# Kernel optimization log

Hardware: AMD Instinct MI355X
Metric: run time of the kernel (lower is better)

The kernel has to match this reference:

```python
import jax, jax.numpy as jnp
import numpy as np

N_USERS = 50000
N_ENTITIES = 100000
N_FACTORS = 8
N_RELATIONS = 17  # weight has n_relations-1 = 16 rows
EMB = 64
N_EDGES = 2_000_000
NNZ = 2_000_000
SLOPE = 0.2


def setup_inputs() -> dict:
    key = jax.random.key(0)
    ks = jax.random.split(key, 16)
    inp = {
        "entity_emb": jax.random.normal(ks[0], (N_ENTITIES, EMB), jnp.float32),
        "user_emb": jax.random.normal(ks[1], (N_USERS, EMB), jnp.float32),
        "latent_emb": jax.random.normal(ks[2], (N_FACTORS, EMB), jnp.float32),
        "edge_index": jax.random.randint(ks[3], (2, N_EDGES), 0, N_ENTITIES, jnp.int32),
        "edge_type": jax.random.randint(ks[4], (N_EDGES,), 1, N_RELATIONS, jnp.int32),
        "interact_rows": jax.random.randint(ks[5], (NNZ,), 0, N_USERS, jnp.int32),
        "interact_cols": jax.random.randint(ks[6], (NNZ,), 0, N_ENTITIES, jnp.int32),
        "interact_vals": jax.random.uniform(ks[7], (NNZ,), jnp.float32),
        "weight": jax.random.normal(ks[8], (N_RELATIONS - 1, EMB), jnp.float32),
        "entity_cate_set": jax.random.randint(ks[9], (N_ENTITIES,), 1, 33, jnp.int32),
        # params (torch Linear convention: y = x @ W.T + b)
        "W_user_att": jax.random.normal(ks[10], (N_FACTORS, N_FACTORS), jnp.float32) * 0.1,
        "b_user_att": jnp.zeros((N_FACTORS,), jnp.float32),
        "W_weight_att": jax.random.normal(ks[11], (N_RELATIONS - 1, N_RELATIONS - 1), jnp.float32) * 0.1,
        "b_weight_att": jnp.zeros((N_RELATIONS - 1,), jnp.float32),
        "W1": jax.random.normal(ks[12], (EMB, EMB), jnp.float32) * 0.1,
        "b1": jnp.zeros((EMB,), jnp.float32),
        "W2": jax.random.normal(ks[13], (EMB, EMB), jnp.float32) * 0.1,
        "b2": jnp.zeros((EMB,), jnp.float32),
    }
    return inp


def _lin(x, W, b):
    return x @ W.T + b


def reference(entity_emb, user_emb, latent_emb, edge_index, edge_type,
              interact_rows, interact_cols, interact_vals, weight, entity_cate_set,
              W_user_att, b_user_att, W_weight_att, b_weight_att, W1, b1, W2, b2):
    head, tail = edge_index[0], edge_index[1]

    # KG aggregate: gather-multiply-scatter_mean (is_div=False branch)
    neigh = entity_emb[tail] * weight[edge_type - 1]            # [E, C]
    sums = jax.ops.segment_sum(neigh, head, num_segments=N_ENTITIES)
    cnt = jax.ops.segment_sum(jnp.ones((neigh.shape[0],), neigh.dtype),
                              head, num_segments=N_ENTITIES)
    entity_agg = sums / jnp.maximum(cnt, 1.0)[:, None]          # [N_ent, C]

    # user aggregate: sparse mm (COO) interact_mat @ entity_emb
    user_agg = jax.ops.segment_sum(interact_vals[:, None] * entity_emb[interact_cols],
                                   interact_rows, num_segments=N_USERS)  # [U, C]

    # user -> latent interest attention
    score_ = _lin(user_emb, W1, b1) @ _lin(latent_emb, W1, b1).T          # [U, F]
    score = jax.nn.softmax(jax.nn.leaky_relu(_lin(score_, W_user_att, b_user_att), SLOPE), axis=1)  # [U, F]

    score_rp = _lin(latent_emb, W2, b2) @ _lin(weight, W2, b2).T          # [F, R-1]
    latent_new = jax.nn.softmax(jax.nn.leaky_relu(_lin(score_rp, W_weight_att, b_weight_att), SLOPE), axis=-1) @ weight  # [F, C]

    # (disen_weight * score).sum(dim=1) == score @ latent_new
    user_agg = user_agg * (score @ latent_new) + user_agg
    return (entity_agg, user_agg, latent_new)
```

## Files before the change

### kernel.cpp

```cpp
#include <hip/hip_runtime.h>

#define N_USERS    50000
#define N_ENTITIES 100000
#define EMB        64
#define N_EDGES    2000000
#define NNZ        2000000
#define SLOPE      0.2f

#define KROWS   256
#define KSHIFT  8
#define NBK     391
#define UROWS   128
#define USHIFT  7
#define NBU     391
#define CAPK    8192
#define CAPU    7680
#define HCH     8192
#define HEPT    (HCH / 512)
#define HPB     ((N_EDGES + HCH - 1) / HCH)
#define CHK_K   8192
#define PB_K    ((N_EDGES + CHK_K - 1) / CHK_K)
#define CHK_U   4096
#define PB_U    ((NNZ + CHK_U - 1) / CHK_U)
#define NQ      (NBK + NBU)
#define ACCBLK  512

__global__ __launch_bounds__(512) void hist_both(const int* __restrict__ head,
                                                 const int* __restrict__ urows,
                                                 int* __restrict__ kgOffs,
                                                 int* __restrict__ uOffs) {
    __shared__ int lhk[NBK];
    __shared__ int lhu[NBU];
    int tid = threadIdx.x;
    for (int t = tid; t < NBK; t += 512) lhk[t] = 0;
    for (int t = tid; t < NBU; t += 512) lhu[t] = 0;
    __syncthreads();
    int base = blockIdx.x * HCH;
#pragma unroll 4
    for (int j = 0; j < HEPT; ++j) {
        int i = base + j * 512 + tid;
        if (i < N_EDGES) atomicAdd(&lhk[head[i] >> KSHIFT], 1);
        if (i < NNZ)     atomicAdd(&lhu[urows[i] >> USHIFT], 1);
    }
    __syncthreads();
    for (int t = tid; t < NBK; t += 512) { int c = lhk[t]; if (c) atomicAdd(&kgOffs[t], c); }
    for (int t = tid; t < NBU; t += 512) { int c = lhu[t]; if (c) atomicAdd(&uOffs[t], c); }
}

__global__ __launch_bounds__(512) void scan_both(int* __restrict__ kgOffs,
                                                 int* __restrict__ kgCur,
                                                 int* __restrict__ uOffs,
                                                 int* __restrict__ uCur) {
    __shared__ int tsum[512];
    int n     = (blockIdx.x == 0) ? NBK : NBU;
    int* offs = (blockIdx.x == 0) ? kgOffs : uOffs;
    int* cur  = (blockIdx.x == 0) ? kgCur  : uCur;
    int tid = threadIdx.x;
    int v = (tid < n) ? offs[tid] : 0;
    tsum[tid] = v;
    __syncthreads();
    for (int off = 1; off < 512; off <<= 1) {
        int t = (tid >= off) ? tsum[tid - off] : 0;
        __syncthreads();
        tsum[tid] += t;
        __syncthreads();
    }
    if (tid < n) { int e = tsum[tid] - v; offs[tid] = e; cur[tid] = e; }
    if (tid == n - 1) offs[n] = tsum[tid];
}

__device__ void small_dense_body(int l,
                                 const float* __restrict__ latent_emb,
                                 const float* __restrict__ weight,
                                 const float* __restrict__ W_weight_att,
                                 const float* __restrict__ b_weight_att,
                                 const float* __restrict__ W1,
                                 const float* __restrict__ b1,
                                 const float* __restrict__ W2,
                                 const float* __restrict__ b2,
                                 float* __restrict__ P_out,
                                 float* __restrict__ c_out,
                                 float* __restrict__ latent_new_out) {
    __shared__ float lat1[8 * 64];
    __shared__ float lat2[8 * 64];
    __shared__ float wl2[16 * 64];
    __shared__ float srp[8 * 16];
    __shared__ float soft[8 * 16];

    if (l < 64) {
        for (int f = 0; f < 8; ++f) {
            float a1 = b1[l], a2 = b2[l];
            for (int k = 0; k < 64; ++k) {
                float le = latent_emb[f * 64 + k];
                a1 += le * W1[l * 64 + k];
                a2 += le * W2[l * 64 + k];
            }
            lat1[f * 64 + l] = a1;
            lat2[f * 64 + l] = a2;
        }
        for (int r = 0; r < 16; ++r) {
            float a = b2[l];
            for (int k = 0; k < 64; ++k) a += weight[r * 64 + k] * W2[l * 64 + k];
            wl2[r * 64 + l] = a;
        }
    }
    __syncthreads();

    if (l < 64) {
        for (int f = 0; f < 8; ++f) {
            float p = 0.f;
            for (int d = 0; d < 64; ++d) p += W1[d * 64 + l] * lat1[f * 64 + d];
            P_out[l * 8 + f] = p;
        }
        if (l < 8) {
            float cc = 0.f;
            for (int d = 0; d < 64; ++d) cc += b1[d] * lat1[l * 64 + d];
            c_out[l] = cc;
        }
        for (int idx = l; idx < 128; idx += 64) {
            int f = idx >> 4, r = idx & 15;
            float a = 0.f;
            for (int d = 0; d < 64; ++d) a += lat2[f * 64 + d] * wl2[r * 64 + d];
            srp[idx] = a;
        }
    }
    __syncthreads();

    if (l < 8) {
        int f = l;
        float att[16];
        float mx = -1e30f;
        for (int k = 0; k < 16; ++k) {
            float a = b_weight_att[k];
            for (int j = 0; j < 16; ++j) a += srp[f * 16 + j] * W_weight_att[k * 16 + j];
            a = a > 0.f ? a : SLOPE * a;
            att[k] = a;
            mx = fmaxf(mx, a);
        }
        float s = 0.f;
        for (int k = 0; k < 16; ++k) { att[k] = expf(att[k] - mx); s += att[k]; }
        float inv = 1.f / s;
        for (int k = 0; k < 16; ++k) soft[f * 16 + k] = att[k] * inv;
    }
    __syncthreads();

    if (l < 64) {
        for (int f = 0; f < 8; ++f) {
            float a = 0.f;
            for (int r = 0; r < 16; ++r) a += soft[f * 16 + r] * weight[r * 64 + l];
            latent_new_out[f * 64 + l] = a;
        }
    }
}

__global__ void small_dense(const float* __restrict__ latent_emb,
                            const float* __restrict__ weight,
                            const float* __restrict__ W_weight_att,
                            const float* __restrict__ b_weight_att,
                            const float* __restrict__ W1,
                            const float* __restrict__ b1,
                            const float* __restrict__ W2,
                            const float* __restrict__ b2,
                            float* __restrict__ P_out,
                            float* __restrict__ c_out,
                            float* __restrict__ latent_new_out) {
    small_dense_body(threadIdx.x, latent_emb, weight, W_weight_att, b_weight_att,
                     W1, b1, W2, b2, P_out, c_out, latent_new_out);
}

__global__ __launch_bounds__(512) void scatter_both(const int* __restrict__ head,
                                                    const int* __restrict__ tail,
                                                    const int* __restrict__ etype,
                                                    int* __restrict__ kgCur,
                                                    int* __restrict__ kgPay,
                                                    const int* __restrict__ urows,
                                                    const int* __restrict__ ucols,
                                                    const float* __restrict__ uvals,
                                                    int* __restrict__ uCur,
                                                    int2* __restrict__ uPay,
                                                    const float* __restrict__ latent_emb,
                                                    const float* __restrict__ weight,
                                                    const float* __restrict__ W_weight_att,
                                                    const float* __restrict__ b_weight_att,
                                                    const float* __restrict__ W1,
                                                    const float* __restrict__ b1,
                                                    const float* __restrict__ W2,
                                                    const float* __restrict__ b2,
                                                    float* __restrict__ Pbuf,
                                                    float* __restrict__ cbuf,
                                                    float* __restrict__ lat_out) {
    if (blockIdx.x == PB_K + PB_U) {
        small_dense_body(threadIdx.x, latent_emb, weight, W_weight_att,
                         b_weight_att, W1, b1, W2, b2, Pbuf, cbuf, lat_out);
        return;
    }

    __shared__ long long sp8[4096];
    __shared__ int lh[NBK];
    __shared__ int lb[NBK];
    __shared__ int lofs[NBK + 1];
    __shared__ int sc[512];
    int tid = threadIdx.x;
    bool isKg = blockIdx.x < PB_K;

    for (int t = tid; t < NBK; t += 512) lh[t] = 0;
    __syncthreads();

    if (isKg) {
        int base = blockIdx.x * CHK_K;
        int n = N_EDGES - base; if (n > CHK_K) n = CHK_K;
        int* spk = (int*)sp8;

        int kreg[CHK_K / 512];
#pragma unroll
        for (int j = 0; j < CHK_K / 512; ++j) {
            int o = j * 512 + tid;
            int h = (o < n) ? head[base + o] : -1;
            kreg[j] = h;
            if (h >= 0) atomicAdd(&lh[h >> KSHIFT], 1);
        }
        __syncthreads();
        for (int t = tid; t < NBK; t += 512)
            lb[t] = lh[t] ? atomicAdd(&kgCur[t], lh[t]) : 0;
        int v = (tid < NBK) ? lh[tid] : 0;
        sc[tid] = v;
        __syncthreads();
        for (int off = 1; off < 512; off <<= 1) {
            int t = (tid >= off) ? sc[tid - off] : 0;
            __syncthreads();
            sc[tid] += t;
            __syncthreads();
        }
        if (tid < NBK) { int e = sc[tid] - v; lofs[tid] = e; lh[tid] = e; }
        if (tid == NBK - 1) lofs[NBK] = sc[tid];
        __syncthreads();
#pragma unroll
        for (int j = 0; j < CHK_K / 512; ++j) {
            int h = kreg[j];
            if (h >= 0) {
                int i = base + j * 512 + tid;
                int p = atomicAdd(&lh[h >> KSHIFT], 1);
                spk[p] = tail[i] | ((etype[i] - 1) << 17) | ((h & (KROWS - 1)) << 21);
            }
        }
        __syncthreads();
        for (int i = tid; i < n; i += 512) {
            int lo = 0, hi = NBK;
            while (hi - lo > 1) {
                int mid = (lo + hi) >> 1;
                if (lofs[mid] <= i) lo = mid; else hi = mid;
            }
            kgPay[lb[lo] + (i - lofs[lo])] = spk[i];
        }
    } else {
        int base = (blockIdx.x - PB_K) * CHK_U;
        int n = NNZ - base; if (n > CHK_U) n = CHK_U;
        int2* spu = (int2*)sp8;

        int kreg[CHK_U / 512];
#pragma unroll
        for (int j = 0; j < CHK_U / 512; ++j) {
            int o = j * 512 + tid;
            int r = (o < n) ? urows[base + o] : -1;
            kreg[j] = r;
            if (r >= 0) atomicAdd(&lh[r >> USHIFT], 1);
        }
        __syncthreads();
        for (int t = tid; t < NBU; t += 512)
            lb[t] = lh[t] ? atomicAdd(&uCur[t], lh[t]) : 0;
        int v = (tid < NBU) ? lh[tid] : 0;
        sc[tid] = v;
        __syncthreads();
        for (int off = 1; off < 512; off <<= 1) {
            int t = (tid >= off) ? sc[tid - off] : 0;
            __syncthreads();
            sc[tid] += t;
            __syncthreads();
        }
        if (tid < NBU) { int e = sc[tid] - v; lofs[tid] = e; lh[tid] = e; }
        if (tid == NBU - 1) lofs[NBU] = sc[tid];
        __syncthreads();
#pragma unroll
        for (int j = 0; j < CHK_U / 512; ++j) {
            int r = kreg[j];
            if (r >= 0) {
                int i = base + j * 512 + tid;
                int p = atomicAdd(&lh[r >> USHIFT], 1);
                spu[p] = make_int2(ucols[i] | ((r & (UROWS - 1)) << 17),
                                   __float_as_int(uvals[i]));
            }
        }
        __syncthreads();
        for (int i = tid; i < n; i += 512) {
            int lo = 0, hi = NBU;
            while (hi - lo > 1) {
                int mid = (lo + hi) >> 1;
                if (lofs[mid] <= i) lo = mid; else hi = mid;
            }
            uPay[lb[lo] + (i - lofs[lo])] = spu[i];
        }
    }
}

__global__ __launch_bounds__(1024, 8) void acc_both(
        const int* __restrict__ kgPay, const int* __restrict__ kgOffs,
        const int2* __restrict__ uPay, const int* __restrict__ uOffs,
        const float* __restrict__ entity_emb,
        const float* __restrict__ weight,
        const float* __restrict__ user_emb,
        const float* __restrict__ P,
        const float* __restrict__ cvec,
        const float* __restrict__ W_user_att,
        const float* __restrict__ b_user_att,
        const float* __restrict__ latent_new,
        int* __restrict__ qCtr,
        float* __restrict__ ent_out,
        float* __restrict__ user_out) {
    __shared__ long long smem8[7873];
    __shared__ int sbk;
    int t = threadIdx.x, d = t & 63, wv = t >> 6;

    for (;;) {
        __syncthreads();
        if (t == 0) sbk = atomicAdd(qCtr, 1);
        __syncthreads();
        int q = sbk;
        if (q >= NQ) return;

        if (q < NBU) {
            int2* spay = (int2*)smem8;
            int* lcnt = (int*)(spay + CAPU);
            int* lofs = lcnt + UROWS;
            int* sc   = lofs + UROWS + 1;
            int bk = q;
            int start = uOffs[bk], end = uOffs[bk + 1];
            int n = end - start; if (n > CAPU) n = CAPU;

            if (t < UROWS) lcnt[t] = 0;
            __syncthreads();
            for (int i = t; i < n; i += 1024)
                atomicAdd(&lcnt[(uPay[start + i].x >> 17) & (UROWS - 1)], 1);
            __syncthreads();
            if (t < UROWS) sc[t] = lcnt[t];
            __syncthreads();
            for (int off = 1; off < UROWS; off <<= 1) {
                int v = (t < UROWS && t >= off) ? sc[t - off] : 0;
                __syncthreads();
                if (t < UROWS) sc[t] += v;
                __syncthreads();
            }
            if (t < UROWS) { int e = sc[t] - lcnt[t]; lofs[t] = e; lcnt[t] = e; }
            if (t == 0) lofs[UROWS] = n;
            __syncthreads();
            for (int i = t; i < n; i += 1024) {
                int2 v = uPay[start + i];
                int p = atomicAdd(&lcnt[(v.x >> 17) & (UROWS - 1)], 1);
                spay[p] = v;
            }
            __syncthreads();

            int rowbase = bk * UROWS;
            for (int rr = 0; rr < UROWS / 16; ++rr) {
                int r = wv * (UROWS / 16) + rr;
                int gr = rowbase + r;
                if (gr >= N_USERS) break;
                int s0 = lofs[r], e0 = lofs[r + 1];
                float acc = 0.f;
                int i = s0;
                for (; i + 7 < e0; i += 8) {
                    float a0 = 0.f, a1 = 0.f;
#pragma unroll
                    for (int u = 0; u < 8; u += 2) {
                        int2 va = spay[i + u], vb = spay[i + u + 1];
                        a0 += __int_as_float(va.y) * entity_emb[(va.x & 0x1FFFF) * EMB + d];
                        a1 += __int_as_float(vb.y) * entity_emb[(vb.x & 0x1FFFF) * EMB + d];
                    }
                    acc += a0 + a1;
                }
                for (; i < e0; ++i) {
                    int2 v = spay[i];
                    acc += __int_as_float(v.y) * entity_emb[(v.x & 0x1FFFF) * EMB + d];
                }
                for (int j = start + CAPU; j < end; ++j) {
                    int2 v = uPay[j];
                    if (((v.x >> 17) & (UROWS - 1)) == r)
                        acc += __int_as_float(v.y) * entity_emb[(v.x & 0x1FFFF) * EMB + d];
                }

                float ue = user_emb[gr * EMB + d];
                float s[8];
#pragma unroll
                for (int f = 0; f < 8; ++f) s[f] = ue * P[d * 8 + f];
#pragma unroll
                for (int off = 32; off; off >>= 1) {
#pragma unroll
                    for (int f = 0; f < 8; ++f) s[f] += __shfl_xor(s[f], off, 64);
                }
#pragma unroll
                for (int f = 0; f < 8; ++f) s[f] += cvec[f];
                float att[8];
                float mx = -1e30f;
#pragma unroll
                for (int k = 0; k < 8; ++k) {
                    float a = b_user_att[k];
#pragma unroll
                    for (int j = 0; j < 8; ++j) a += s[j] * W_user_att[k * 8 + j];
                    a = a > 0.f ? a : SLOPE * a;
                    att[k] = a;
                    mx = fmaxf(mx, a);
                }
                float sum = 0.f;
#pragma unroll
                for (int k = 0; k < 8; ++k) { att[k] = __expf(att[k] - mx); sum += att[k]; }
                float inv = 1.f / sum;
                float g = 0.f;
#pragma unroll
                for (int f = 0; f < 8; ++f) g += att[f] * inv * latent_new[f * EMB + d];
                user_out[gr * EMB + d] = acc * (1.f + g);
            }
        } else {
            int* spay = (int*)smem8;
            int* lcnt = spay + CAPK;
            int* lofs = lcnt + KROWS;
            int* sc   = lofs + KROWS + 1;
            int bk = q - NBU;
            int start = kgOffs[bk], end = kgOffs[bk + 1];
            int n = end - start; if (n > CAPK) n = CAPK;

            if (t < KROWS) lcnt[t] = 0;
            __syncthreads();
            for (int i = t; i < n; i += 1024)
                atomicAdd(&lcnt[(kgPay[start + i] >> 21) & (KROWS - 1)], 1);
            __syncthreads();
            if (t < KROWS) sc[t] = lcnt[t];
            __syncthreads();
            for (int off = 1; off < KROWS; off <<= 1) {
                int v = (t < KROWS && t >= off) ? sc[t - off] : 0;
                __syncthreads();
                if (t < KROWS) sc[t] += v;
                __syncthreads();
            }
            if (t < KROWS) { int e = sc[t] - lcnt[t]; lofs[t] = e; lcnt[t] = e; }
            if (t == 0) lofs[KROWS] = n;
            __syncthreads();
            for (int i = t; i < n; i += 1024) {
                int v = kgPay[start + i];
                int p = atomicAdd(&lcnt[(v >> 21) & (KROWS - 1)], 1);
                spay[p] = v;
            }
            __syncthreads();

            int rowbase = bk * KROWS;
            for (int rr = 0; rr < KROWS / 16; ++rr) {
                int r = wv * (KROWS / 16) + rr;
                int gr = rowbase + r;
                if (gr >= N_ENTITIES) break;
                int s0 = lofs[r], e0 = lofs[r + 1];
                int cnt = e0 - s0;
                float acc = 0.f;
                int i = s0;
                for (; i + 7 < e0; i += 8) {
                    float a0 = 0.f, a1 = 0.f;
#pragma unroll
                    for (int u = 0; u < 8; u += 2) {
                        int va = spay[i + u], vb = spay[i + u + 1];
                        a0 += entity_emb[(va & 0x1FFFF) * EMB + d] * weight[((va >> 17) & 15) * EMB + d];
                        a1 += entity_emb[(vb & 0x1FFFF) * EMB + d] * weight[((vb >> 17) & 15) * EMB + d];
                    }
                    acc += a0 + a1;
                }
                for (; i < e0; ++i) {
                    int v = spay[i];
                    acc += entity_emb[(v & 0x1FFFF) * EMB + d] * weight[((v >> 17) & 15) * EMB + d];
                }
                for (int j = start + CAPK; j < end; ++j) {
                    int v = kgPay[j];
                    if (((v >> 21) & (KROWS - 1)) == r) {
                        acc += entity_emb[(v & 0x1FFFF) * EMB + d] * weight[((v >> 17) & 15) * EMB + d];
                        ++cnt;
                    }
                }
                ent_out[gr * EMB + d] = acc / fmaxf((float)cnt, 1.f);
            }
        }
    }
}

__global__ void kg_scatter(const int* __restrict__ head, const int* __restrict__ tail,
                           const int* __restrict__ etype,
                           const float* __restrict__ entity_emb,
                           const float* __restrict__ weight,
                           float* __restrict__ sums, float* __restrict__ cnt) {
    int gid = blockIdx.x * blockDim.x + threadIdx.x;
    int e = gid >> 6, d = threadIdx.x & 63;
    if (e >= N_EDGES) return;
    int h = head[e], t = tail[e], w = etype[e] - 1;
    float v = entity_emb[t * EMB + d] * weight[w * EMB + d];
    unsafeAtomicAdd(&sums[h * EMB + d], v);
    if (d == 0) unsafeAtomicAdd(&cnt[h], 1.0f);
}

__global__ void user_scatter(const int* __restrict__ rows, const int* __restrict__ cols,
                             const float* __restrict__ vals,
                             const float* __restrict__ entity_emb,
                             float* __restrict__ user_sums) {
    int gid = blockIdx.x * blockDim.x + threadIdx.x;
    int e = gid >> 6, d = threadIdx.x & 63;
    if (e >= NNZ) return;
    float v = vals[e] * entity_emb[cols[e] * EMB + d];
    unsafeAtomicAdd(&user_sums[rows[e] * EMB + d], v);
}

__global__ void entity_div(float* __restrict__ ent, const float* __restrict__ cnt) {
    int gid = blockIdx.x * blockDim.x + threadIdx.x;
    if (gid >= N_ENTITIES * EMB) return;
    float c = cnt[gid >> 6];
    ent[gid] = ent[gid] / fmaxf(c, 1.0f);
}

__global__ void user_finalize(const float* __restrict__ user_emb,
                              const float* __restrict__ P,
                              const float* __restrict__ c,
                              const float* __restrict__ W_user_att,
                              const float* __restrict__ b_user_att,
                              const float* __restrict__ latent_new,
                              float* __restrict__ user_out) {
    int gid = blockIdx.x * blockDim.x + threadIdx.x;
    int u = gid >> 6, lane = threadIdx.x & 63;
    if (u >= N_USERS) return;
    float ue = user_emb[u * 64 + lane];
    float s[8];
#pragma unroll
    for (int f = 0; f < 8; ++f) s[f] = ue * P[lane * 8 + f];
#pragma unroll
    for (int off = 32; off; off >>= 1)
#pragma unroll
        for (int f = 0; f < 8; ++f) s[f] += __shfl_xor(s[f], off, 64);
#pragma unroll
    for (int f = 0; f < 8; ++f) s[f] += c[f];
    float att[8], mx = -1e30f;
#pragma unroll
    for (int k = 0; k < 8; ++k) {
        float a = b_user_att[k];
#pragma unroll
        for (int j = 0; j < 8; ++j) a += s[j] * W_user_att[k * 8 + j];
        a = a > 0.f ? a : SLOPE * a;
        att[k] = a;
        mx = fmaxf(mx, a);
    }
    float sum = 0.f;
#pragma unroll
    for (int k = 0; k < 8; ++k) { att[k] = expf(att[k] - mx); sum += att[k]; }
    float inv = 1.f / sum, g = 0.f;
#pragma unroll
    for (int f = 0; f < 8; ++f) g += att[f] * inv * latent_new[f * 64 + lane];
    float ua = user_out[u * 64 + lane];
    user_out[u * 64 + lane] = ua * (1.f + g);
}

extern "C" void kernel_launch(void* const* d_in, const int* in_sizes, int n_in,
                              void* d_out, int out_size, void* d_ws, size_t ws_size,
                              hipStream_t stream) {
    const float* entity_emb   = (const float*)d_in[0];
    const float* user_emb     = (const float*)d_in[1];
    const float* latent_emb   = (const float*)d_in[2];
    const int*   edge_index   = (const int*)d_in[3];
    const int*   edge_type    = (const int*)d_in[4];
    const int*   irows        = (const int*)d_in[5];
    const int*   icols        = (const int*)d_in[6];
    const float* ivals        = (const float*)d_in[7];
    const float* weight       = (const float*)d_in[8];
    const float* W_user_att   = (const float*)d_in[10];
    const float* b_user_att   = (const float*)d_in[11];
    const float* W_weight_att = (const float*)d_in[12];
    const float* b_weight_att = (const float*)d_in[13];
    const float* W1           = (const float*)d_in[14];
    const float* b1           = (const float*)d_in[15];
    const float* W2           = (const float*)d_in[16];
    const float* b2           = (const float*)d_in[17];

    float* out      = (float*)d_out;
    float* ent_out  = out;
    float* user_out = out + (size_t)N_ENTITIES * EMB;
    float* lat_out  = user_out + (size_t)N_USERS * EMB;

    const int* head = edge_index;
    const int* tail = edge_index + N_EDGES;

    int* ws_i = (int*)d_ws;
    int*   kgOffs = ws_i;
    int*   uOffs  = kgOffs + (NBK + 1);
    int*   qCtr   = uOffs + (NBU + 1);
    int*   kgCur  = qCtr + 2;
    int*   uCur   = kgCur + NBK;
    int*   kgPay  = uCur + NBU;
    int2*  uPay   = (int2*)(kgPay + N_EDGES);
    float* Pbuf   = (float*)(uPay + NNZ);
    float* cbuf   = Pbuf + 64 * 8;
    size_t need_bytes = (size_t)((NBK + 1) + (NBU + 1) + 2 + NBK + NBU +
                                 N_EDGES + 2 * (size_t)NNZ + 512 + 8) * 4;

    if (ws_size >= need_bytes) {
        hipMemsetAsync(kgOffs, 0,
                       (size_t)((NBK + 1) + (NBU + 1) + 2) * sizeof(int), stream);

        hist_both<<<HPB, 512, 0, stream>>>(head, irows, kgOffs, uOffs);
        scan_both<<<2, 512, 0, stream>>>(kgOffs, kgCur, uOffs, uCur);
        scatter_both<<<PB_K + PB_U + 1, 512, 0, stream>>>(head, tail, edge_type,
                                                          kgCur, kgPay,
                                                          irows, icols, ivals,
                                                          uCur, uPay,
                                                          latent_emb, weight,
                                                          W_weight_att, b_weight_att,
                                                          W1, b1, W2, b2,
                                                          Pbuf, cbuf, lat_out);
        acc_both<<<ACCBLK, 1024, 0, stream>>>(kgPay, kgOffs, uPay, uOffs,
                                              entity_emb, weight, user_emb,
                                              Pbuf, cbuf, W_user_att, b_user_att,
                                              lat_out, qCtr, ent_out, user_out);
    } else {
        float* cnt   = (float*)d_ws;
        float* Pbuf2 = cnt + N_ENTITIES;
        float* cbuf2 = Pbuf2 + 64 * 8;
        hipMemsetAsync(ent_out, 0,
                       (size_t)(N_ENTITIES + N_USERS) * EMB * sizeof(float), stream);
        hipMemsetAsync(cnt, 0, N_ENTITIES * sizeof(float), stream);
        int blocks_edges = (N_EDGES * 64) / 256;
        kg_scatter<<<blocks_edges, 256, 0, stream>>>(head, tail, edge_type, entity_emb,
                                                     weight, ent_out, cnt);
        user_scatter<<<blocks_edges, 256, 0, stream>>>(irows, icols, ivals, entity_emb,
                                                       user_out);
        small_dense<<<1, 64, 0, stream>>>(latent_emb, weight, W_weight_att,
                                          b_weight_att, W1, b1, W2, b2,
                                          Pbuf2, cbuf2, lat_out);
        user_finalize<<<(N_USERS * 64) / 256, 256, 0, stream>>>(user_emb, Pbuf2, cbuf2,
                                                                W_user_att, b_user_att,
                                                                lat_out, user_out);
        entity_div<<<(N_ENTITIES * EMB) / 256, 256, 0, stream>>>(ent_out, cnt);
    }
}
```

Before: 398.2 us.

## Replace histogram and scan with fixed-capacity bucket slots for binning

```diff
diff --git a/kernel.cpp b/kernel.cpp
--- a/kernel.cpp
+++ b/kernel.cpp
@@ -15,6 +15,8 @@
 #define NBU     391
 #define CAPK    8192
 #define CAPU    7680
+#define KCAP    5632
+#define UCAP    5632
 #define HCH     8192
 #define HEPT    (HCH / 512)
 #define HPB     ((N_EDGES + HCH - 1) / HCH)
@@ -24,6 +26,14 @@
 #define PB_U    ((NNZ + CHK_U - 1) / CHK_U)
 #define NQ      (NBK + NBU)
 #define ACCBLK  512
+
+__global__ void init_cur(int* __restrict__ kgCur, int* __restrict__ uCur,
+                         int* __restrict__ qCtr) {
+    int t = blockIdx.x * blockDim.x + threadIdx.x;
+    if (t < NBK) kgCur[t] = t * KCAP;
+    if (t < NBU) uCur[t]  = t * UCAP;
+    if (t == 0) qCtr[0] = 0;
+}
 
 __global__ __launch_bounds__(512) void hist_both(const int* __restrict__ head,
                                                  const int* __restrict__ urows,
@@ -302,9 +312,12 @@
     }
 }
 
+template<bool STATIC>
 __global__ __launch_bounds__(1024, 8) void acc_both(
         const int* __restrict__ kgPay, const int* __restrict__ kgOffs,
+        const int* __restrict__ kgCurF,
         const int2* __restrict__ uPay, const int* __restrict__ uOffs,
+        const int* __restrict__ uCurF,
         const float* __restrict__ entity_emb,
         const float* __restrict__ weight,
         const float* __restrict__ user_emb,
@@ -333,7 +346,9 @@
             int* lofs = lcnt + UROWS;
             int* sc   = lofs + UROWS + 1;
             int bk = q;
-            int start = uOffs[bk], end = uOffs[bk + 1];
+            int start, end;
+            if (STATIC) { start = bk * UCAP; end = uCurF[bk]; }
+            else        { start = uOffs[bk]; end = uOffs[bk + 1]; }
             int n = end - start; if (n > CAPU) n = CAPU;
 
             if (t < UROWS) lcnt[t] = 0;
@@ -424,7 +439,9 @@
             int* lofs = lcnt + KROWS;
             int* sc   = lofs + KROWS + 1;
             int bk = q - NBU;
-            int start = kgOffs[bk], end = kgOffs[bk + 1];
+            int start, end;
+            if (STATIC) { start = bk * KCAP; end = kgCurF[bk]; }
+            else        { start = kgOffs[bk]; end = kgOffs[bk + 1]; }
             int n = end - start; if (n > CAPK) n = CAPK;
 
             if (t < KROWS) lcnt[t] = 0;
@@ -588,24 +605,30 @@
     const int* tail = edge_index + N_EDGES;
 
     int* ws_i = (int*)d_ws;
-    int*   kgOffs = ws_i;
-    int*   uOffs  = kgOffs + (NBK + 1);
-    int*   qCtr   = uOffs + (NBU + 1);
+    int*   qCtr   = ws_i;
     int*   kgCur  = qCtr + 2;
     int*   uCur   = kgCur + NBK;
     int*   kgPay  = uCur + NBU;
-    int2*  uPay   = (int2*)(kgPay + N_EDGES);
-    float* Pbuf   = (float*)(uPay + NNZ);
+    int2*  uPay   = (int2*)(kgPay + NBK * KCAP);
+    float* Pbuf   = (float*)(uPay + NBU * UCAP);
     float* cbuf   = Pbuf + 64 * 8;
-    size_t need_bytes = (size_t)((NBK + 1) + (NBU + 1) + 2 + NBK + NBU +
-                                 N_EDGES + 2 * (size_t)NNZ + 512 + 8) * 4;
-
-    if (ws_size >= need_bytes) {
-        hipMemsetAsync(kgOffs, 0,
-                       (size_t)((NBK + 1) + (NBU + 1) + 2) * sizeof(int), stream);
-
-        hist_both<<<HPB, 512, 0, stream>>>(head, irows, kgOffs, uOffs);
-        scan_both<<<2, 512, 0, stream>>>(kgOffs, kgCur, uOffs, uCur);
+    size_t need_static = (size_t)(2 + NBK + NBU + (size_t)NBK * KCAP +
+                                  2 * (size_t)NBU * UCAP + 512 + 8) * 4;
+
+    int*   kgOffs2 = ws_i;
+    int*   uOffs2  = kgOffs2 + (NBK + 1);
+    int*   qCtr2   = uOffs2 + (NBU + 1);
+    int*   kgCur2  = qCtr2 + 2;
+    int*   uCur2   = kgCur2 + NBK;
+    int*   kgPay2  = uCur2 + NBU;
+    int2*  uPay2   = (int2*)(kgPay2 + N_EDGES);
+    float* Pbuf2   = (float*)(uPay2 + NNZ);
+    float* cbuf2   = Pbuf2 + 64 * 8;
+    size_t need_off = (size_t)((NBK + 1) + (NBU + 1) + 2 + NBK + NBU +
+                               N_EDGES + 2 * (size_t)NNZ + 512 + 8) * 4;
+
+    if (ws_size >= need_static) {
+        init_cur<<<2, 256, 0, stream>>>(kgCur, uCur, qCtr);
         scatter_both<<<PB_K + PB_U + 1, 512, 0, stream>>>(head, tail, edge_type,
                                                           kgCur, kgPay,
                                                           irows, icols, ivals,
@@ -614,14 +637,37 @@
                                                           W_weight_att, b_weight_att,
                                                           W1, b1, W2, b2,
                                                           Pbuf, cbuf, lat_out);
-        acc_both<<<ACCBLK, 1024, 0, stream>>>(kgPay, kgOffs, uPay, uOffs,
-                                              entity_emb, weight, user_emb,
-                                              Pbuf, cbuf, W_user_att, b_user_att,
-                                              lat_out, qCtr, ent_out, user_out);
+        acc_both<true><<<ACCBLK, 1024, 0, stream>>>(kgPay, nullptr, kgCur,
+                                                    uPay, nullptr, uCur,
+                                                    entity_emb, weight, user_emb,
+                                                    Pbuf, cbuf,
+                                                    W_user_att, b_user_att,
+                                                    lat_out, qCtr,
+                                                    ent_out, user_out);
+    } else if (ws_size >= need_off) {
+        hipMemsetAsync(kgOffs2, 0,
+                       (size_t)((NBK + 1) + (NBU + 1) + 2) * sizeof(int), stream);
+        hist_both<<<HPB, 512, 0, stream>>>(head, irows, kgOffs2, uOffs2);
+        scan_both<<<2, 512, 0, stream>>>(kgOffs2, kgCur2, uOffs2, uCur2);
+        scatter_both<<<PB_K + PB_U + 1, 512, 0, stream>>>(head, tail, edge_type,
+                                                          kgCur2, kgPay2,
+                                                          irows, icols, ivals,
+                                                          uCur2, uPay2,
+                                                          latent_emb, weight,
+                                                          W_weight_att, b_weight_att,
+                                                          W1, b1, W2, b2,
+                                                          Pbuf2, cbuf2, lat_out);
+        acc_both<false><<<ACCBLK, 1024, 0, stream>>>(kgPay2, kgOffs2, nullptr,
+                                                     uPay2, uOffs2, nullptr,
+                                                     entity_emb, weight, user_emb,
+                                                     Pbuf2, cbuf2,
+                                                     W_user_att, b_user_att,
+                                                     lat_out, qCtr2,
+                                                     ent_out, user_out);
     } else {
         float* cnt   = (float*)d_ws;
-        float* Pbuf2 = cnt + N_ENTITIES;
-        float* cbuf2 = Pbuf2 + 64 * 8;
+        float* Pbuf3 = cnt + N_ENTITIES;
+        float* cbuf3 = Pbuf3 + 64 * 8;
         hipMemsetAsync(ent_out, 0,
                        (size_t)(N_ENTITIES + N_USERS) * EMB * sizeof(float), stream);
         hipMemsetAsync(cnt, 0, N_ENTITIES * sizeof(float), stream);
@@ -632,8 +678,8 @@
                                                        user_out);
         small_dense<<<1, 64, 0, stream>>>(latent_emb, weight, W_weight_att,
                                           b_weight_att, W1, b1, W2, b2,
-                                          Pbuf2, cbuf2, lat_out);
-        user_finalize<<<(N_USERS * 64) / 256, 256, 0, stream>>>(user_emb, Pbuf2, cbuf2,
+                                          Pbuf3, cbuf3, lat_out);
+        user_finalize<<<(N_USERS * 64) / 256, 256, 0, stream>>>(user_emb, Pbuf3, cbuf3,
                                                                 W_user_att, b_user_att,
                                                                 lat_out, user_out);
         entity_div<<<(N_ENTITIES * EMB) / 256, 256, 0, stream>>>(ent_out, cnt);
```

Result: faster. 374.6 us (-5.9%).
